# Performance work log

Measured on AMD Instinct MI355X. Metric: run time of the kernel, lower is better.

The kernel has to match this reference:

```python
import jax, jax.numpy as jnp
import numpy as np

NB_CLASSES = 10
EPS = 1e-8  # torch cosine_similarity eps


def gcn_conv(x, W, b, src, dst, n):
    h = x @ W
    deg = jax.ops.segment_sum(jnp.ones_like(src, dtype=h.dtype), dst, num_segments=n) + 1.0
    dinv = deg ** -0.5
    coef = (dinv[src] * dinv[dst])[:, None]
    agg = jax.ops.segment_sum(h[src] * coef, dst, num_segments=n)
    return agg + h * (1.0 / deg)[:, None] + b


def condition_net(e, w_in, b_in, w_hid, b_hid, w_out, b_out):
    # ConditionNet with num_layers=2: input_fc -> elu -> hidden_fc[0] -> elu -> output_fc
    h = jax.nn.elu(e @ w_in + b_in)
    h = jax.nn.elu(h @ w_hid + b_hid)
    return h @ w_out + b_out


def setup_inputs() -> dict:
    key = jax.random.key(0)
    N, E, D, H, T, M = 20000, 320000, 256, 256, 3, 2048
    ks = jax.random.split(key, 24)
    s = 1.0 / np.sqrt(D)
    inp = {
        "x": jax.random.normal(ks[0], (N, D), dtype=jnp.float32),
        "src": jax.random.randint(ks[1], (E,), 0, N, dtype=jnp.int32),
        "dst": jax.random.randint(ks[2], (E,), 0, N, dtype=jnp.int32),
        "idx": jax.random.randint(ks[3], (M,), 0, N, dtype=jnp.int32),
        "labels": jax.random.randint(ks[4], (M,), 0, NB_CLASSES, dtype=jnp.int32),
        "train": 1,
        # 3 GCNConv layers (all D->D, residual structure forces equal widths)
        "gcn_W1": jax.random.normal(ks[5], (D, D), dtype=jnp.float32) * s,
        "gcn_b1": jnp.zeros((D,), dtype=jnp.float32),
        "gcn_W2": jax.random.normal(ks[6], (D, D), dtype=jnp.float32) * s,
        "gcn_b2": jnp.zeros((D,), dtype=jnp.float32),
        "gcn_W3": jax.random.normal(ks[7], (D, D), dtype=jnp.float32) * s,
        "gcn_b3": jnp.zeros((D,), dtype=jnp.float32),
        # T=3 ConditionNets, params stacked on leading axis
        "cn_w_in": jax.random.normal(ks[8], (T, D, H), dtype=jnp.float32) * s,
        "cn_b_in": jnp.zeros((T, H), dtype=jnp.float32),
        "cn_w_hid": jax.random.normal(ks[9], (T, H, H), dtype=jnp.float32) * s,
        "cn_b_hid": jnp.zeros((T, H), dtype=jnp.float32),
        "cn_w_out": jax.random.normal(ks[10], (T, H, D), dtype=jnp.float32) * s,
        "cn_b_out": jnp.zeros((T, D), dtype=jnp.float32),
        # Embed_prompt
        "p_list": jax.random.normal(ks[11], (5, D), dtype=jnp.float32) * s,
        "a_W": jax.random.normal(ks[12], (D, 5), dtype=jnp.float32) * s,
        "a_b": jnp.zeros((5,), dtype=jnp.float32),
        # gcn_weight2 (trainable); weight1 and weight3 are frozen zeros, closed over
        "gcn_weight2": jnp.float32(1.0),
    }
    return inp


def reference(x, src, dst, idx, labels, train,
              gcn_W1, gcn_b1, gcn_W2, gcn_b2, gcn_W3, gcn_b3,
              cn_w_in, cn_b_in, cn_w_hid, cn_b_hid, cn_w_out, cn_b_out,
              p_list, a_W, a_b, gcn_weight2):
    n = x.shape[0]
    origin_x = x
    w1 = jnp.float32(0.0)  # gcn_weight1 (frozen)
    w3 = jnp.float32(0.0)  # gcn_weight3 (frozen)
    T = cn_w_in.shape[0]
    for t in range(T):  # think layers (small static count)
        e1 = gcn_conv(x, gcn_W1, gcn_b1, src, dst, n)
        e2 = gcn_conv(e1, gcn_W2, gcn_b2, src, dst, n) + e1
        e3 = gcn_conv(e2, gcn_W3, gcn_b3, src, dst, n) + e2
        embed = w1 * e1 + gcn_weight2 * e2 + w3 * e3
        prompt = condition_net(embed, cn_w_in[t], cn_b_in[t], cn_w_hid[t], cn_b_hid[t],
                               cn_w_out[t], cn_b_out[t])
        x = prompt * origin_x
    # full gcn(x, edge_index): 3 convs with ELU activation (standard GCN forward)
    h = jax.nn.elu(gcn_conv(x, gcn_W1, gcn_b1, src, dst, n))
    h = jax.nn.elu(gcn_conv(h, gcn_W2, gcn_b2, src, dst, n))
    h = jax.nn.elu(gcn_conv(h, gcn_W3, gcn_b3, src, dst, n))
    # Embed_prompt: attention over 5 learned prompt vectors
    weight = jax.nn.softmax(h @ a_W + a_b, axis=1)  # [N, 5]
    embed = h + weight @ p_list
    rawret = embed[idx]  # [M, D]
    # train==1: class prototypes via scatter-mean over labels
    sums = jax.ops.segment_sum(rawret, labels, num_segments=NB_CLASSES)
    counts = jax.ops.segment_sum(jnp.ones_like(labels, dtype=rawret.dtype), labels,
                                 num_segments=NB_CLASSES)
    ave = sums / jnp.maximum(counts, 1.0)[:, None]  # [C, D]
    # fused cosine similarity: normalize both, one matmul (replaces M*C scalar loop)
    rn = rawret / jnp.maximum(jnp.linalg.norm(rawret, axis=1, keepdims=True), EPS)
    an = ave / jnp.maximum(jnp.linalg.norm(ave, axis=1, keepdims=True), EPS)
    ret = jax.nn.softmax(rn @ an.T, axis=1)  # [M, C]
    return ret
```

## Files before the change

### kernel.cpp

```cpp
#include <hip/hip_runtime.h>
#include <hip/hip_bf16.h>
#include <math.h>

#define NN 20000
#define DD 256
#define EE 320000
#define MM 2048
#define CC 10
#define TT 3

typedef __attribute__((ext_vector_type(8))) short s8v;
typedef __attribute__((ext_vector_type(4))) float f4v;

__device__ unsigned short g_xb[NN * DD];
__device__ unsigned short g_xo[NN * DD];
__device__ unsigned short g_hb[NN * DD];
__device__ unsigned short g_e1b[NN * DD];
__device__ unsigned short g_e2b[NN * DD];
__device__ int   g_cnt[NN];
__device__ int   g_cursor[NN];
__device__ int   g_rowstart[NN + 1];
__device__ float g_dinv[NN];
__device__ float g_invdeg[NN];
__device__ int   g_part[128];
__device__ int2  g_edge[EE];
__device__ float g_sums[CC * DD];
__device__ float g_cntf[CC];
__device__ float g_an[CC * DD];
__device__ unsigned short g_wT1[12 * DD * DD];
__device__ unsigned short g_wT2[12 * DD * DD];

__device__ __forceinline__ float wave_sum(float v) {
#pragma unroll
  for (int off = 32; off > 0; off >>= 1) v += __shfl_xor(v, off);
  return v;
}

__device__ __forceinline__ float eluf(float x) {
  return x > 0.f ? x : expm1f(x);
}

__device__ __forceinline__ float bf2f(unsigned short u) {
  union { unsigned int i; float f; } c;
  c.i = (unsigned int)u << 16;
  return c.f;
}

__device__ __forceinline__ float2 bfpair(unsigned int d) {
  union { unsigned int i; float f; } a, b;
  a.i = d << 16;
  b.i = d & 0xffff0000u;
  return make_float2(a.f, b.f);
}

__device__ __forceinline__ unsigned int packbf(float x, float y) {
  union { __hip_bfloat162 v; unsigned int u; } c;
  c.v = __float22bfloat162_rn(make_float2(x, y));
  return c.u;
}

__device__ __forceinline__ void gl_lds16(const unsigned short* g, unsigned short* l) {
  __builtin_amdgcn_global_load_lds(
      (const __attribute__((address_space(1))) unsigned int*)g,
      (__attribute__((address_space(3))) unsigned int*)l, 16, 0, 0);
}

__global__ void zero_pre() {
  int i = blockIdx.x * blockDim.x + threadIdx.x;
  if (i < NN) { g_cnt[i] = 0; g_cursor[i] = 0; }
  if (i < CC * DD) g_sums[i] = 0.f;
  if (i < CC) g_cntf[i] = 0.f;
}

__global__ void hist_k(const int* __restrict__ dst) {
  int e = blockIdx.x * blockDim.x + threadIdx.x;
  if (e < EE) atomicAdd(&g_cnt[dst[e]], 1);
}

__global__ __launch_bounds__(256) void scanA_k() {
  __shared__ int s[256];
  int t = threadIdx.x;
  int i = blockIdx.x * 256 + t;
  int v = (i < NN) ? g_cnt[i] : 0;
  s[t] = v;
  __syncthreads();
#pragma unroll
  for (int off = 128; off > 0; off >>= 1) {
    if (t < off) s[t] += s[t + off];
    __syncthreads();
  }
  if (t == 0) g_part[blockIdx.x] = s[0];
}

__global__ __launch_bounds__(128) void scanB_k() {
  __shared__ int s[128];
  int t = threadIdx.x;
  int p = (t < 79) ? g_part[t] : 0;
  s[t] = p;
  __syncthreads();
#pragma unroll
  for (int off = 1; off < 128; off <<= 1) {
    int v = (t >= off) ? s[t - off] : 0;
    __syncthreads();
    s[t] += v;
    __syncthreads();
  }
  g_part[t] = s[t] - p;
  if (t == 0) g_rowstart[NN] = EE;
}

__global__ __launch_bounds__(256) void scanC_k() {
  __shared__ int s[256];
  int t = threadIdx.x;
  int i = blockIdx.x * 256 + t;
  int v = (i < NN) ? g_cnt[i] : 0;
  s[t] = v;
  __syncthreads();
#pragma unroll
  for (int off = 1; off < 256; off <<= 1) {
    int x = (t >= off) ? s[t - off] : 0;
    __syncthreads();
    s[t] += x;
    __syncthreads();
  }
  if (i < NN) {
    g_rowstart[i] = g_part[blockIdx.x] + s[t] - v;
    float dg = (float)(v + 1);
    g_invdeg[i] = 1.0f / dg;
    g_dinv[i] = 1.0f / sqrtf(dg);
  }
}

__global__ void fill_k(const int* __restrict__ src, const int* __restrict__ dst) {
  int e = blockIdx.x * blockDim.x + threadIdx.x;
  if (e < EE) {
    int d = dst[e];
    int p = atomicAdd(&g_cursor[d], 1);
    int j = g_rowstart[d] + p;
    int si = src[e];
    float coef = g_dinv[si] * g_dinv[d];
    g_edge[j] = make_int2(si * 512, __float_as_int(coef));
  }
}

__global__ __launch_bounds__(256) void cvt_k(const float* __restrict__ x,
                                             unsigned short* __restrict__ xb) {
  int i = blockIdx.x * blockDim.x + threadIdx.x;
  const float4* x4 = (const float4*)x;
  float4 a = x4[i * 2], b = x4[i * 2 + 1];
  uint4 o;
  o.x = packbf(a.x, a.y);
  o.y = packbf(a.z, a.w);
  o.z = packbf(b.x, b.y);
  o.w = packbf(b.z, b.w);
  ((uint4*)xb)[i] = o;
}

struct WPtrs { const float* p[12]; };

__global__ __launch_bounds__(256) void wprep_k(WPtrs wp) {
  __shared__ float t[64][65];
  int widx = blockIdx.z;
  int kt0 = blockIdx.x * 64, nt0 = blockIdx.y * 64;
  const float* W = wp.p[widx];
  int tid = threadIdx.x;
  int ln = tid & 63, lk = tid >> 6;
  for (int kk = lk; kk < 64; kk += 4)
    t[kk][ln] = W[(size_t)(kt0 + kk) * DD + nt0 + ln];
  __syncthreads();
  for (int nn = lk; nn < 64; nn += 4) {
    float v = t[ln][nn];
    __hip_bfloat16 hb = __float2bfloat16(v);
    float hf = __bfloat162float(hb);
    __hip_bfloat16 lb = __float2bfloat16(v - hf);
    union { __hip_bfloat16 b; unsigned short s; } ch, cl;
    ch.b = hb; cl.b = lb;
    size_t o = (size_t)widx * DD * DD + (size_t)(nt0 + nn) * DD + kt0 + ln;
    g_wT1[o] = ch.s;
    g_wT2[o] = cl.s;
  }
}

template <int SPLIT>
union GemmSM {
  unsigned short st[2][(1024 + 512 * SPLIT) * 8];
  float ct[64][68];
};

template <int EPI, int SPLIT>
__global__ __launch_bounds__(256) void gemm_k(const unsigned short* __restrict__ A,
                                              const unsigned short* __restrict__ B1,
                                              const unsigned short* __restrict__ B2,
                                              unsigned short* __restrict__ C,
                                              const float* __restrict__ bias,
                                              const float* __restrict__ alphap,
                                              const unsigned short* __restrict__ mul) {
  __shared__ GemmSM<SPLIT> sm;
  constexpr int CB = 1024 + 512 * SPLIT;
  int b = blockIdx.x;
  int xcd = b & 7, off = b >> 3;
  int logical = (xcd < 4) ? xcd * 157 + off : 628 + (xcd - 4) * 156 + off;
  int mblk = logical >> 2, nblk = logical & 3;
  int row0 = mblk * 64, col0 = nblk * 64;

  int tid = threadIdx.x;
  int wv = tid >> 6, lane = tid & 63;
  int wm = wv >> 1, wn = wv & 1;
  int lr = lane & 15, lk = lane >> 4;

  f4v acc[2][2];
#pragma unroll
  for (int i = 0; i < 2; ++i)
#pragma unroll
    for (int j = 0; j < 2; ++j) acc[i][j] = (f4v){0.f, 0.f, 0.f, 0.f};

  auto stage = [&](int buf, int kt) {
    unsigned short* base = sm.st[buf];
#pragma unroll
    for (int i = 0; i < CB / 256; ++i) {
      int cb = (wv * (CB / 256) + i) * 64;
      int c = cb + lane;
      unsigned short* ldst = base + (size_t)cb * 8;
      if (c < 512) {
        int row = c >> 3, pos = c & 7;
        int kc = pos ^ (row & 7);
        int gr = row0 + row;
        gr = gr < NN ? gr : NN - 1;
        gl_lds16(A + (size_t)gr * DD + kt + kc * 8, ldst);
      } else if (c < 1024) {
        int c2 = c - 512;
        int col = c2 >> 3, pos = c2 & 7;
        int kc = pos ^ (col & 7);
        gl_lds16(B1 + (size_t)(col0 + col) * DD + kt + kc * 8, ldst);
      } else {
        int c2 = c - 1024;
        int col = c2 >> 3, pos = c2 & 7;
        int kc = pos ^ (col & 7);
        gl_lds16(B2 + (size_t)(col0 + col) * DD + kt + kc * 8, ldst);
      }
    }
  };

  stage(0, 0);
  __syncthreads();

  int buf = 0;
#pragma unroll
  for (int t = 0; t < 4; ++t) {
    if (t < 3) stage(buf ^ 1, (t + 1) * 64);
    const unsigned short* base = sm.st[buf];
#pragma unroll
    for (int ksub = 0; ksub < 2; ++ksub) {
      int kc = ksub * 4 + lk;
      s8v a[2], b1v[2], b2v[2];
#pragma unroll
      for (int mi = 0; mi < 2; ++mi) {
        int row = wm * 32 + mi * 16 + lr;
        a[mi] = *(const s8v*)(base + (row * 8 + (kc ^ (row & 7))) * 8);
      }
#pragma unroll
      for (int nj = 0; nj < 2; ++nj) {
        int col = wn * 32 + nj * 16 + lr;
        int ch = col * 8 + (kc ^ (col & 7));
        b1v[nj] = *(const s8v*)(base + (512 + ch) * 8);
        if (SPLIT) b2v[nj] = *(const s8v*)(base + (1024 + ch) * 8);
      }
#pragma unroll
      for (int mi = 0; mi < 2; ++mi)
#pragma unroll
        for (int nj = 0; nj < 2; ++nj) {
          acc[mi][nj] = __builtin_amdgcn_mfma_f32_16x16x32_bf16(a[mi], b1v[nj], acc[mi][nj], 0, 0, 0);
          if (SPLIT)
            acc[mi][nj] = __builtin_amdgcn_mfma_f32_16x16x32_bf16(a[mi], b2v[nj], acc[mi][nj], 0, 0, 0);
        }
    }
    __syncthreads();
    buf ^= 1;
  }

#pragma unroll
  for (int mi = 0; mi < 2; ++mi)
#pragma unroll
    for (int nj = 0; nj < 2; ++nj)
#pragma unroll
      for (int r = 0; r < 4; ++r)
        sm.ct[wm * 32 + mi * 16 + lk * 4 + r][wn * 32 + nj * 16 + lr] = acc[mi][nj][r];
  __syncthreads();

  float alpha = 1.f;
  if (EPI == 1) alpha = alphap ? *alphap : 1.f;
#pragma unroll
  for (int p = 0; p < 2; ++p) {
    int row = p * 32 + (tid >> 3);
    int c0 = (tid & 7) * 8;
    int gr = row0 + row;
    int gc = col0 + c0;
    if (gr < NN) {
      float v[8];
      float4 va = *(float4*)&sm.ct[row][c0];
      float4 vb = *(float4*)&sm.ct[row][c0 + 4];
      v[0] = va.x; v[1] = va.y; v[2] = va.z; v[3] = va.w;
      v[4] = vb.x; v[5] = vb.y; v[6] = vb.z; v[7] = vb.w;
      if (EPI == 1) {
        float4 bv0 = *(const float4*)(bias + gc);
        float4 bv1 = *(const float4*)(bias + gc + 4);
        float bb[8] = {bv0.x, bv0.y, bv0.z, bv0.w, bv1.x, bv1.y, bv1.z, bv1.w};
#pragma unroll
        for (int i = 0; i < 8; ++i) v[i] = eluf(fmaf(alpha, v[i], bb[i]));
      } else if (EPI == 2) {
        float4 bv0 = *(const float4*)(bias + gc);
        float4 bv1 = *(const float4*)(bias + gc + 4);
        float bb[8] = {bv0.x, bv0.y, bv0.z, bv0.w, bv1.x, bv1.y, bv1.z, bv1.w};
        uint4 mu = *(const uint4*)(mul + (size_t)gr * DD + gc);
        float2 m0 = bfpair(mu.x), m1 = bfpair(mu.y), m2 = bfpair(mu.z), m3 = bfpair(mu.w);
        float mm[8] = {m0.x, m0.y, m1.x, m1.y, m2.x, m2.y, m3.x, m3.y};
#pragma unroll
        for (int i = 0; i < 8; ++i) v[i] = (v[i] + bb[i]) * mm[i];
      }
      uint4 o;
      o.x = packbf(v[0], v[1]);
      o.y = packbf(v[2], v[3]);
      o.z = packbf(v[4], v[5]);
      o.w = packbf(v[6], v[7]);
      *(uint4*)(C + (size_t)gr * DD + gc) = o;
    }
  }
}

template <int RES>
__device__ __forceinline__ float4 agg_row_b(int row, int lane,
                                            const unsigned short* __restrict__ h,
                                            const float* __restrict__ bias,
                                            const unsigned short* __restrict__ res) {
  const char* hb = (const char*)h;
  int lo = lane * 8;
  float4 a = make_float4(0.f, 0.f, 0.f, 0.f);
  int s = g_rowstart[row], e = g_rowstart[row + 1];
  int j = s;
  for (; j + 16 <= e; j += 16) {
    int2 E[16];
    uint2 v[16];
#pragma unroll
    for (int u = 0; u < 16; ++u) E[u] = g_edge[j + u];
#pragma unroll
    for (int u = 0; u < 16; ++u) v[u] = *(const uint2*)(hb + E[u].x + lo);
#pragma unroll
    for (int u = 0; u < 16; ++u) {
      float c = __int_as_float(E[u].y);
      float2 p0 = bfpair(v[u].x), p1 = bfpair(v[u].y);
      a.x = fmaf(c, p0.x, a.x); a.y = fmaf(c, p0.y, a.y);
      a.z = fmaf(c, p1.x, a.z); a.w = fmaf(c, p1.y, a.w);
    }
  }
  for (; j + 4 <= e; j += 4) {
    int2 E[4];
    uint2 v[4];
#pragma unroll
    for (int u = 0; u < 4; ++u) E[u] = g_edge[j + u];
#pragma unroll
    for (int u = 0; u < 4; ++u) v[u] = *(const uint2*)(hb + E[u].x + lo);
#pragma unroll
    for (int u = 0; u < 4; ++u) {
      float c = __int_as_float(E[u].y);
      float2 p0 = bfpair(v[u].x), p1 = bfpair(v[u].y);
      a.x = fmaf(c, p0.x, a.x); a.y = fmaf(c, p0.y, a.y);
      a.z = fmaf(c, p1.x, a.z); a.w = fmaf(c, p1.y, a.w);
    }
  }
  for (; j < e; ++j) {
    int2 E0 = g_edge[j];
    uint2 v0 = *(const uint2*)(hb + E0.x + lo);
    float c = __int_as_float(E0.y);
    float2 p0 = bfpair(v0.x), p1 = bfpair(v0.y);
    a.x = fmaf(c, p0.x, a.x); a.y = fmaf(c, p0.y, a.y);
    a.z = fmaf(c, p1.x, a.z); a.w = fmaf(c, p1.y, a.w);
  }
  float idg = g_invdeg[row];
  uint2 hv = *(const uint2*)(hb + row * 512 + lo);
  float2 h0 = bfpair(hv.x), h1 = bfpair(hv.y);
  float4 bv = ((const float4*)bias)[lane];
  float4 o;
  o.x = a.x + h0.x * idg + bv.x;
  o.y = a.y + h0.y * idg + bv.y;
  o.z = a.z + h1.x * idg + bv.z;
  o.w = a.w + h1.y * idg + bv.w;
  if (RES) {
    uint2 rv = *(const uint2*)((const char*)res + row * 512 + lo);
    float2 r0 = bfpair(rv.x), r1 = bfpair(rv.y);
    o.x += r0.x; o.y += r0.y; o.z += r1.x; o.w += r1.y;
  }
  return o;
}

template <int ELU, int RES>
__global__ __launch_bounds__(256) void agg_k(const unsigned short* __restrict__ h,
                                             const float* __restrict__ bias,
                                             const unsigned short* __restrict__ res,
                                             unsigned short* __restrict__ out) {
  int row = (blockIdx.x * 256 + threadIdx.x) >> 6;
  int lane = threadIdx.x & 63;
  float4 o = agg_row_b<RES>(row, lane, h, bias, res);
  if (ELU) {
    o.x = eluf(o.x); o.y = eluf(o.y); o.z = eluf(o.z); o.w = eluf(o.w);
  }
  ((uint2*)out)[(size_t)row * 64 + lane] = make_uint2(packbf(o.x, o.y), packbf(o.z, o.w));
}

__global__ __launch_bounds__(256) void aggattn_k(const unsigned short* __restrict__ h,
                                                 const float* __restrict__ bias,
                                                 const float* __restrict__ aW,
                                                 const float* __restrict__ ab,
                                                 const float* __restrict__ plist,
                                                 unsigned short* __restrict__ out) {
  int row = (blockIdx.x * 256 + threadIdx.x) >> 6;
  int lane = threadIdx.x & 63;
  float4 o = agg_row_b<0>(row, lane, h, bias, nullptr);
  o.x = eluf(o.x); o.y = eluf(o.y); o.z = eluf(o.z); o.w = eluf(o.w);
  int d = lane * 4;
  float lg[5];
#pragma unroll
  for (int k = 0; k < 5; ++k) {
    float p = o.x * aW[(d + 0) * 5 + k] + o.y * aW[(d + 1) * 5 + k] +
              o.z * aW[(d + 2) * 5 + k] + o.w * aW[(d + 3) * 5 + k];
    lg[k] = wave_sum(p) + ab[k];
  }
  float mx = lg[0];
#pragma unroll
  for (int k = 1; k < 5; ++k) mx = fmaxf(mx, lg[k]);
  float w[5], sum = 0.f;
#pragma unroll
  for (int k = 0; k < 5; ++k) { w[k] = expf(lg[k] - mx); sum += w[k]; }
  float inv = 1.f / sum;
#pragma unroll
  for (int k = 0; k < 5; ++k) {
    float wk = w[k] * inv;
    float4 pv = ((const float4*)plist)[k * 64 + lane];
    o.x = fmaf(wk, pv.x, o.x);
    o.y = fmaf(wk, pv.y, o.y);
    o.z = fmaf(wk, pv.z, o.z);
    o.w = fmaf(wk, pv.w, o.w);
  }
  ((uint2*)out)[(size_t)row * 64 + lane] = make_uint2(packbf(o.x, o.y), packbf(o.z, o.w));
}

__global__ __launch_bounds__(256) void proto_k(const unsigned short* __restrict__ embed,
                                               const int* __restrict__ idxp,
                                               const int* __restrict__ labels) {
  __shared__ float sums[CC][DD];
  __shared__ float cnts[CC];
  int t = threadIdx.x;
#pragma unroll
  for (int c = 0; c < CC; ++c) sums[c][t] = 0.f;
  if (t < CC) cnts[t] = 0.f;
  __syncthreads();
  int m0 = blockIdx.x * 32;
  for (int r0 = 0; r0 < 32; r0 += 4) {
    int i4[4], l4[4];
    float v[4];
#pragma unroll
    for (int u = 0; u < 4; ++u) {
      int m = m0 + r0 + u;
      i4[u] = idxp[m];
      l4[u] = labels[m];
    }
#pragma unroll
    for (int u = 0; u < 4; ++u) v[u] = bf2f(embed[(size_t)i4[u] * DD + t]);
#pragma unroll
    for (int u = 0; u < 4; ++u) sums[l4[u]][t] += v[u];
    if (t == 0) {
#pragma unroll
      for (int u = 0; u < 4; ++u) cnts[l4[u]] += 1.f;
    }
  }
  __syncthreads();
#pragma unroll
  for (int c = 0; c < CC; ++c) atomicAdd(&g_sums[c * DD + t], sums[c][t]);
  if (t < CC) atomicAdd(&g_cntf[t], cnts[t]);
}

__global__ void protonorm_k() {
  __shared__ float red[4];
  int t = threadIdx.x;
  int lane = t & 63, w = t >> 6;
  for (int c = 0; c < CC; ++c) {
    float v = g_sums[c * DD + t] / fmaxf(g_cntf[c], 1.0f);
    float sq = wave_sum(v * v);
    if (lane == 0) red[w] = sq;
    __syncthreads();
    float tot = red[0] + red[1] + red[2] + red[3];
    float nrm = fmaxf(sqrtf(tot), 1e-8f);
    g_an[c * DD + t] = v / nrm;
    __syncthreads();
  }
}

__global__ __launch_bounds__(256) void cos_k(const unsigned short* __restrict__ embed,
                                             const int* __restrict__ idxp,
                                             float* __restrict__ out) {
  int wid = (blockIdx.x * 256 + threadIdx.x) >> 6;
  int lane = threadIdx.x & 63;
  if (wid >= MM) return;
  int row = idxp[wid];
  uint2 rv = ((const uint2*)embed)[(size_t)row * 64 + lane];
  float2 r0 = bfpair(rv.x), r1 = bfpair(rv.y);
  float4 r = make_float4(r0.x, r0.y, r1.x, r1.y);
  float n = wave_sum(r.x * r.x + r.y * r.y + r.z * r.z + r.w * r.w);
  float rnf = 1.0f / fmaxf(sqrtf(n), 1e-8f);
  float lg[CC];
#pragma unroll
  for (int c = 0; c < CC; ++c) {
    float4 a = ((const float4*)g_an)[c * 64 + lane];
    float p = r.x * a.x + r.y * a.y + r.z * a.z + r.w * a.w;
    lg[c] = wave_sum(p) * rnf;
  }
  float mx = lg[0];
#pragma unroll
  for (int c = 1; c < CC; ++c) mx = fmaxf(mx, lg[c]);
  float s = 0.f, w[CC];
#pragma unroll
  for (int c = 0; c < CC; ++c) { w[c] = expf(lg[c] - mx); s += w[c]; }
  float inv = 1.f / s;
#pragma unroll
  for (int c = 0; c < CC; ++c)
    if (lane == c) out[(size_t)wid * CC + c] = w[c] * inv;
}

extern "C" void kernel_launch(void* const* d_in, const int* in_sizes, int n_in,
                              void* d_out, int out_size, void* d_ws, size_t ws_size,
                              hipStream_t stream) {
  (void)in_sizes; (void)n_in; (void)d_ws; (void)ws_size; (void)out_size;
  const float* x      = (const float*)d_in[0];
  const int*   src    = (const int*)d_in[1];
  const int*   dst    = (const int*)d_in[2];
  const int*   idx    = (const int*)d_in[3];
  const int*   labels = (const int*)d_in[4];
  const float* W1 = (const float*)d_in[6];
  const float* b1 = (const float*)d_in[7];
  const float* W2 = (const float*)d_in[8];
  const float* b2 = (const float*)d_in[9];
  const float* W3 = (const float*)d_in[10];
  const float* b3 = (const float*)d_in[11];
  const float* cw_in  = (const float*)d_in[12];
  const float* cb_in  = (const float*)d_in[13];
  const float* cw_hid = (const float*)d_in[14];
  const float* cb_hid = (const float*)d_in[15];
  const float* cw_out = (const float*)d_in[16];
  const float* cb_out = (const float*)d_in[17];
  const float* plist  = (const float*)d_in[18];
  const float* aW     = (const float*)d_in[19];
  const float* ab     = (const float*)d_in[20];
  const float* w2s    = (const float*)d_in[21];
  float* out = (float*)d_out;

  unsigned short *xb, *xo, *hb, *e1b, *e2b, *wt1, *wt2;
  hipGetSymbolAddress((void**)&xb,  HIP_SYMBOL(g_xb));
  hipGetSymbolAddress((void**)&xo,  HIP_SYMBOL(g_xo));
  hipGetSymbolAddress((void**)&hb,  HIP_SYMBOL(g_hb));
  hipGetSymbolAddress((void**)&e1b, HIP_SYMBOL(g_e1b));
  hipGetSymbolAddress((void**)&e2b, HIP_SYMBOL(g_e2b));
  hipGetSymbolAddress((void**)&wt1, HIP_SYMBOL(g_wT1));
  hipGetSymbolAddress((void**)&wt2, HIP_SYMBOL(g_wT2));

  auto WT1 = [&](int w) { return (const unsigned short*)(wt1 + (size_t)w * DD * DD); };
  auto WT2 = [&](int w) { return (const unsigned short*)(wt2 + (size_t)w * DD * DD); };

  zero_pre<<<79, 256, 0, stream>>>();
  hist_k<<<1250, 256, 0, stream>>>(dst);
  scanA_k<<<79, 256, 0, stream>>>();
  scanB_k<<<1, 128, 0, stream>>>();
  scanC_k<<<79, 256, 0, stream>>>();
  fill_k<<<1250, 256, 0, stream>>>(src, dst);
  cvt_k<<<2500, 256, 0, stream>>>(x, xb);

  WPtrs wp;
  wp.p[0] = W1; wp.p[1] = W2; wp.p[2] = W3;
  for (int t = 0; t < 3; ++t) {
    wp.p[3 + t] = cw_in  + (size_t)t * DD * DD;
    wp.p[6 + t] = cw_hid + (size_t)t * DD * DD;
    wp.p[9 + t] = cw_out + (size_t)t * DD * DD;
  }
  wprep_k<<<dim3(4, 4, 12), 256, 0, stream>>>(wp);

  const int GG = 1252;
  const unsigned short* xin = xb;
  for (int t = 0; t < TT; ++t) {
    gemm_k<0, 1><<<GG, 256, 0, stream>>>(xin, WT1(0), WT2(0), hb, nullptr, nullptr, nullptr);
    agg_k<0, 0><<<5000, 256, 0, stream>>>(hb, b1, nullptr, e1b);
    gemm_k<0, 1><<<GG, 256, 0, stream>>>(e1b, WT1(1), WT2(1), hb, nullptr, nullptr, nullptr);
    agg_k<0, 1><<<5000, 256, 0, stream>>>(hb, b2, e1b, e2b);
    gemm_k<1, 0><<<GG, 256, 0, stream>>>(e2b, WT1(3 + t), WT1(3 + t), e1b,
                                         cb_in + (size_t)t * DD, w2s, nullptr);
    gemm_k<1, 0><<<GG, 256, 0, stream>>>(e1b, WT1(6 + t), WT1(6 + t), hb,
                                         cb_hid + (size_t)t * DD, nullptr, nullptr);
    gemm_k<2, 0><<<GG, 256, 0, stream>>>(hb, WT1(9 + t), WT1(9 + t), xo,
                                         cb_out + (size_t)t * DD, nullptr, xb);
    xin = xo;
  }

  gemm_k<0, 1><<<GG, 256, 0, stream>>>(xin, WT1(0), WT2(0), hb, nullptr, nullptr, nullptr);
  agg_k<1, 0><<<5000, 256, 0, stream>>>(hb, b1, nullptr, e1b);
  gemm_k<0, 1><<<GG, 256, 0, stream>>>(e1b, WT1(1), WT2(1), hb, nullptr, nullptr, nullptr);
  agg_k<1, 0><<<5000, 256, 0, stream>>>(hb, b2, nullptr, e2b);
  gemm_k<0, 1><<<GG, 256, 0, stream>>>(e2b, WT1(2), WT2(2), hb, nullptr, nullptr, nullptr);
  aggattn_k<<<5000, 256, 0, stream>>>(hb, b3, aW, ab, plist, e2b);

  proto_k<<<64, 256, 0, stream>>>(e2b, idx, labels);
  protonorm_k<<<1, 256, 0, stream>>>();
  cos_k<<<512, 256, 0, stream>>>(e2b, idx, out);
}
```

Before: 579.8 us.

## Fuse setup kernels, fold scan and protonorm, widen aggregation gathers to 16 bytes

Merges the zero, bf16 conversion and weight-prep kernels into one init kernel. It folds the single-block partial-sum scan into scanC and the prototype normalization into cos_k, which cuts several launches. The SpMM aggregation now splits each wave into two half-waves that each gather 16-byte row slices for alternating edges and combine them with a shuffle, so each load is wider and half as many row segments are fetched per lane. Each cos block recomputes the prototype norms redundantly, and the odd-edge tail uses a clamped index with a zero coefficient.

```diff
diff --git a/kernel.cpp b/kernel.cpp
--- a/kernel.cpp
+++ b/kernel.cpp
@@ -26,7 +26,6 @@
 __device__ int2  g_edge[EE];
 __device__ float g_sums[CC * DD];
 __device__ float g_cntf[CC];
-__device__ float g_an[CC * DD];
 __device__ unsigned short g_wT1[12 * DD * DD];
 __device__ unsigned short g_wT2[12 * DD * DD];
 
@@ -65,11 +64,51 @@
       (__attribute__((address_space(3))) unsigned int*)l, 16, 0, 0);
 }
 
-__global__ void zero_pre() {
-  int i = blockIdx.x * blockDim.x + threadIdx.x;
-  if (i < NN) { g_cnt[i] = 0; g_cursor[i] = 0; }
-  if (i < CC * DD) g_sums[i] = 0.f;
-  if (i < CC) g_cntf[i] = 0.f;
+struct WPtrs { const float* p[12]; };
+
+__global__ __launch_bounds__(256) void init_k(const float* __restrict__ x,
+                                              unsigned short* __restrict__ xb,
+                                              WPtrs wp) {
+  __shared__ float t[64][65];
+  int b = blockIdx.x;
+  int tid = threadIdx.x;
+  if (b < 2500) {
+    int i = b * 256 + tid;
+    const float4* x4 = (const float4*)x;
+    float4 a = x4[i * 2], bb = x4[i * 2 + 1];
+    uint4 o;
+    o.x = packbf(a.x, a.y);
+    o.y = packbf(a.z, a.w);
+    o.z = packbf(bb.x, bb.y);
+    o.w = packbf(bb.z, bb.w);
+    ((uint4*)xb)[i] = o;
+  } else if (b < 2692) {
+    int bb = b - 2500;
+    int widx = bb >> 4;
+    int rem = bb & 15;
+    int kt0 = (rem >> 2) * 64, nt0 = (rem & 3) * 64;
+    const float* W = wp.p[widx];
+    int ln = tid & 63, lk = tid >> 6;
+    for (int kk = lk; kk < 64; kk += 4)
+      t[kk][ln] = W[(size_t)(kt0 + kk) * DD + nt0 + ln];
+    __syncthreads();
+    for (int nn = lk; nn < 64; nn += 4) {
+      float v = t[ln][nn];
+      __hip_bfloat16 hb = __float2bfloat16(v);
+      float hf = __bfloat162float(hb);
+      __hip_bfloat16 lb = __float2bfloat16(v - hf);
+      union { __hip_bfloat16 b; unsigned short s; } ch, cl;
+      ch.b = hb; cl.b = lb;
+      size_t o = (size_t)widx * DD * DD + (size_t)(nt0 + nn) * DD + kt0 + ln;
+      g_wT1[o] = ch.s;
+      g_wT2[o] = cl.s;
+    }
+  } else {
+    int i = (b - 2692) * 256 + tid;
+    if (i < NN) { g_cnt[i] = 0; g_cursor[i] = 0; }
+    if (i < CC * DD) g_sums[i] = 0.f;
+    if (i < CC) g_cntf[i] = 0.f;
+  }
 }
 
 __global__ void hist_k(const int* __restrict__ dst) {
@@ -92,43 +131,38 @@
   if (t == 0) g_part[blockIdx.x] = s[0];
 }
 
-__global__ __launch_bounds__(128) void scanB_k() {
-  __shared__ int s[128];
-  int t = threadIdx.x;
-  int p = (t < 79) ? g_part[t] : 0;
-  s[t] = p;
-  __syncthreads();
-#pragma unroll
-  for (int off = 1; off < 128; off <<= 1) {
-    int v = (t >= off) ? s[t - off] : 0;
-    __syncthreads();
-    s[t] += v;
-    __syncthreads();
-  }
-  g_part[t] = s[t] - p;
-  if (t == 0) g_rowstart[NN] = EE;
-}
-
 __global__ __launch_bounds__(256) void scanC_k() {
+  __shared__ int ps[128];
   __shared__ int s[256];
   int t = threadIdx.x;
+  if (t < 128) ps[t] = (t < 79) ? g_part[t] : 0;
+  __syncthreads();
+#pragma unroll
+  for (int off = 1; off < 128; off <<= 1) {
+    int v = (t >= off && t < 128) ? ps[t - off] : 0;
+    __syncthreads();
+    if (t < 128) ps[t] += v;
+    __syncthreads();
+  }
+  int base = (blockIdx.x == 0) ? 0 : ps[blockIdx.x - 1];
   int i = blockIdx.x * 256 + t;
   int v = (i < NN) ? g_cnt[i] : 0;
   s[t] = v;
   __syncthreads();
 #pragma unroll
   for (int off = 1; off < 256; off <<= 1) {
-    int x = (t >= off) ? s[t - off] : 0;
-    __syncthreads();
-    s[t] += x;
+    int x2 = (t >= off) ? s[t - off] : 0;
+    __syncthreads();
+    s[t] += x2;
     __syncthreads();
   }
   if (i < NN) {
-    g_rowstart[i] = g_part[blockIdx.x] + s[t] - v;
+    g_rowstart[i] = base + s[t] - v;
     float dg = (float)(v + 1);
     g_invdeg[i] = 1.0f / dg;
     g_dinv[i] = 1.0f / sqrtf(dg);
   }
+  if (blockIdx.x == 78 && t == 0) g_rowstart[NN] = EE;
 }
 
 __global__ void fill_k(const int* __restrict__ src, const int* __restrict__ dst) {
@@ -140,44 +174,6 @@
     int si = src[e];
     float coef = g_dinv[si] * g_dinv[d];
     g_edge[j] = make_int2(si * 512, __float_as_int(coef));
-  }
-}
-
-__global__ __launch_bounds__(256) void cvt_k(const float* __restrict__ x,
-                                             unsigned short* __restrict__ xb) {
-  int i = blockIdx.x * blockDim.x + threadIdx.x;
-  const float4* x4 = (const float4*)x;
-  float4 a = x4[i * 2], b = x4[i * 2 + 1];
-  uint4 o;
-  o.x = packbf(a.x, a.y);
-  o.y = packbf(a.z, a.w);
-  o.z = packbf(b.x, b.y);
-  o.w = packbf(b.z, b.w);
-  ((uint4*)xb)[i] = o;
-}
-
-struct WPtrs { const float* p[12]; };
-
-__global__ __launch_bounds__(256) void wprep_k(WPtrs wp) {
-  __shared__ float t[64][65];
-  int widx = blockIdx.z;
-  int kt0 = blockIdx.x * 64, nt0 = blockIdx.y * 64;
-  const float* W = wp.p[widx];
-  int tid = threadIdx.x;
-  int ln = tid & 63, lk = tid >> 6;
-  for (int kk = lk; kk < 64; kk += 4)
-    t[kk][ln] = W[(size_t)(kt0 + kk) * DD + nt0 + ln];
-  __syncthreads();
-  for (int nn = lk; nn < 64; nn += 4) {
-    float v = t[ln][nn];
-    __hip_bfloat16 hb = __float2bfloat16(v);
-    float hf = __bfloat162float(hb);
-    __hip_bfloat16 lb = __float2bfloat16(v - hf);
-    union { __hip_bfloat16 b; unsigned short s; } ch, cl;
-    ch.b = hb; cl.b = lb;
-    size_t o = (size_t)widx * DD * DD + (size_t)(nt0 + nn) * DD + kt0 + ln;
-    g_wT1[o] = ch.s;
-    g_wT2[o] = cl.s;
   }
 }
 
@@ -328,68 +324,67 @@
 }
 
 template <int RES>
-__device__ __forceinline__ float4 agg_row_b(int row, int lane,
-                                            const unsigned short* __restrict__ h,
-                                            const float* __restrict__ bias,
-                                            const unsigned short* __restrict__ res) {
+__device__ __forceinline__ void agg_row8(int row, int sl, int hf,
+                                         const unsigned short* __restrict__ h,
+                                         const float* __restrict__ bias,
+                                         const unsigned short* __restrict__ res,
+                                         float* o) {
   const char* hb = (const char*)h;
-  int lo = lane * 8;
-  float4 a = make_float4(0.f, 0.f, 0.f, 0.f);
+  int lo = sl * 16;
+  float acc[8];
+#pragma unroll
+  for (int k = 0; k < 8; ++k) acc[k] = 0.f;
   int s = g_rowstart[row], e = g_rowstart[row + 1];
   int j = s;
-  for (; j + 16 <= e; j += 16) {
-    int2 E[16];
-    uint2 v[16];
-#pragma unroll
-    for (int u = 0; u < 16; ++u) E[u] = g_edge[j + u];
-#pragma unroll
-    for (int u = 0; u < 16; ++u) v[u] = *(const uint2*)(hb + E[u].x + lo);
-#pragma unroll
-    for (int u = 0; u < 16; ++u) {
+  for (; j + 12 <= e; j += 12) {
+    int2 E[6];
+    uint4 V[6];
+#pragma unroll
+    for (int u = 0; u < 6; ++u) E[u] = g_edge[j + 2 * u + hf];
+#pragma unroll
+    for (int u = 0; u < 6; ++u) V[u] = *(const uint4*)(hb + (size_t)E[u].x + lo);
+#pragma unroll
+    for (int u = 0; u < 6; ++u) {
       float c = __int_as_float(E[u].y);
-      float2 p0 = bfpair(v[u].x), p1 = bfpair(v[u].y);
-      a.x = fmaf(c, p0.x, a.x); a.y = fmaf(c, p0.y, a.y);
-      a.z = fmaf(c, p1.x, a.z); a.w = fmaf(c, p1.y, a.w);
+      float2 p0 = bfpair(V[u].x), p1 = bfpair(V[u].y);
+      float2 p2 = bfpair(V[u].z), p3 = bfpair(V[u].w);
+      acc[0] = fmaf(c, p0.x, acc[0]); acc[1] = fmaf(c, p0.y, acc[1]);
+      acc[2] = fmaf(c, p1.x, acc[2]); acc[3] = fmaf(c, p1.y, acc[3]);
+      acc[4] = fmaf(c, p2.x, acc[4]); acc[5] = fmaf(c, p2.y, acc[5]);
+      acc[6] = fmaf(c, p3.x, acc[6]); acc[7] = fmaf(c, p3.y, acc[7]);
     }
   }
-  for (; j + 4 <= e; j += 4) {
-    int2 E[4];
-    uint2 v[4];
-#pragma unroll
-    for (int u = 0; u < 4; ++u) E[u] = g_edge[j + u];
-#pragma unroll
-    for (int u = 0; u < 4; ++u) v[u] = *(const uint2*)(hb + E[u].x + lo);
-#pragma unroll
-    for (int u = 0; u < 4; ++u) {
-      float c = __int_as_float(E[u].y);
-      float2 p0 = bfpair(v[u].x), p1 = bfpair(v[u].y);
-      a.x = fmaf(c, p0.x, a.x); a.y = fmaf(c, p0.y, a.y);
-      a.z = fmaf(c, p1.x, a.z); a.w = fmaf(c, p1.y, a.w);
-    }
-  }
-  for (; j < e; ++j) {
-    int2 E0 = g_edge[j];
-    uint2 v0 = *(const uint2*)(hb + E0.x + lo);
-    float c = __int_as_float(E0.y);
-    float2 p0 = bfpair(v0.x), p1 = bfpair(v0.y);
-    a.x = fmaf(c, p0.x, a.x); a.y = fmaf(c, p0.y, a.y);
-    a.z = fmaf(c, p1.x, a.z); a.w = fmaf(c, p1.y, a.w);
-  }
+  for (; j < e; j += 2) {
+    int jj = j + hf;
+    int jc = jj < e ? jj : e - 1;
+    int2 E0 = g_edge[jc];
+    uint4 V0 = *(const uint4*)(hb + (size_t)E0.x + lo);
+    float c = (jj < e) ? __int_as_float(E0.y) : 0.f;
+    float2 p0 = bfpair(V0.x), p1 = bfpair(V0.y);
+    float2 p2 = bfpair(V0.z), p3 = bfpair(V0.w);
+    acc[0] = fmaf(c, p0.x, acc[0]); acc[1] = fmaf(c, p0.y, acc[1]);
+    acc[2] = fmaf(c, p1.x, acc[2]); acc[3] = fmaf(c, p1.y, acc[3]);
+    acc[4] = fmaf(c, p2.x, acc[4]); acc[5] = fmaf(c, p2.y, acc[5]);
+    acc[6] = fmaf(c, p3.x, acc[6]); acc[7] = fmaf(c, p3.y, acc[7]);
+  }
+#pragma unroll
+  for (int k = 0; k < 8; ++k) acc[k] += __shfl_xor(acc[k], 32);
   float idg = g_invdeg[row];
-  uint2 hv = *(const uint2*)(hb + row * 512 + lo);
-  float2 h0 = bfpair(hv.x), h1 = bfpair(hv.y);
-  float4 bv = ((const float4*)bias)[lane];
-  float4 o;
-  o.x = a.x + h0.x * idg + bv.x;
-  o.y = a.y + h0.y * idg + bv.y;
-  o.z = a.z + h1.x * idg + bv.z;
-  o.w = a.w + h1.y * idg + bv.w;
+  uint4 hv = *(const uint4*)(hb + (size_t)row * 512 + lo);
+  float2 h0 = bfpair(hv.x), h1 = bfpair(hv.y), h2 = bfpair(hv.z), h3 = bfpair(hv.w);
+  float hw[8] = {h0.x, h0.y, h1.x, h1.y, h2.x, h2.y, h3.x, h3.y};
+  float4 b0 = *(const float4*)(bias + sl * 8);
+  float4 b1 = *(const float4*)(bias + sl * 8 + 4);
+  float bb[8] = {b0.x, b0.y, b0.z, b0.w, b1.x, b1.y, b1.z, b1.w};
+#pragma unroll
+  for (int k = 0; k < 8; ++k) o[k] = acc[k] + hw[k] * idg + bb[k];
   if (RES) {
-    uint2 rv = *(const uint2*)((const char*)res + row * 512 + lo);
-    float2 r0 = bfpair(rv.x), r1 = bfpair(rv.y);
-    o.x += r0.x; o.y += r0.y; o.z += r1.x; o.w += r1.y;
-  }
-  return o;
+    uint4 rv = *(const uint4*)((const char*)res + (size_t)row * 512 + lo);
+    float2 r0 = bfpair(rv.x), r1 = bfpair(rv.y), r2 = bfpair(rv.z), r3 = bfpair(rv.w);
+    float rw[8] = {r0.x, r0.y, r1.x, r1.y, r2.x, r2.y, r3.x, r3.y};
+#pragma unroll
+    for (int k = 0; k < 8; ++k) o[k] += rw[k];
+  }
 }
 
 template <int ELU, int RES>
@@ -399,11 +394,21 @@
                                              unsigned short* __restrict__ out) {
   int row = (blockIdx.x * 256 + threadIdx.x) >> 6;
   int lane = threadIdx.x & 63;
-  float4 o = agg_row_b<RES>(row, lane, h, bias, res);
+  int sl = lane & 31, hf = lane >> 5;
+  float o[8];
+  agg_row8<RES>(row, sl, hf, h, bias, res, o);
   if (ELU) {
-    o.x = eluf(o.x); o.y = eluf(o.y); o.z = eluf(o.z); o.w = eluf(o.w);
-  }
-  ((uint2*)out)[(size_t)row * 64 + lane] = make_uint2(packbf(o.x, o.y), packbf(o.z, o.w));
+#pragma unroll
+    for (int k = 0; k < 8; ++k) o[k] = eluf(o[k]);
+  }
+  if (hf == 0) {
+    uint4 pk;
+    pk.x = packbf(o[0], o[1]);
+    pk.y = packbf(o[2], o[3]);
+    pk.z = packbf(o[4], o[5]);
+    pk.w = packbf(o[6], o[7]);
+    *(uint4*)((char*)out + (size_t)row * 512 + sl * 16) = pk;
+  }
 }
 
 __global__ __launch_bounds__(256) void aggattn_k(const unsigned short* __restrict__ h,
@@ -414,15 +419,19 @@
                                                  unsigned short* __restrict__ out) {
   int row = (blockIdx.x * 256 + threadIdx.x) >> 6;
   int lane = threadIdx.x & 63;
-  float4 o = agg_row_b<0>(row, lane, h, bias, nullptr);
-  o.x = eluf(o.x); o.y = eluf(o.y); o.z = eluf(o.z); o.w = eluf(o.w);
-  int d = lane * 4;
+  int sl = lane & 31, hf = lane >> 5;
+  float o[8];
+  agg_row8<0>(row, sl, hf, h, bias, nullptr, o);
+#pragma unroll
+  for (int k = 0; k < 8; ++k) o[k] = eluf(o[k]);
+  int c0 = sl * 8;
   float lg[5];
 #pragma unroll
   for (int k = 0; k < 5; ++k) {
-    float p = o.x * aW[(d + 0) * 5 + k] + o.y * aW[(d + 1) * 5 + k] +
-              o.z * aW[(d + 2) * 5 + k] + o.w * aW[(d + 3) * 5 + k];
-    lg[k] = wave_sum(p) + ab[k];
+    float p = 0.f;
+#pragma unroll
+    for (int i = 0; i < 8; ++i) p = fmaf(o[i], aW[(c0 + i) * 5 + k], p);
+    lg[k] = wave_sum(p) * 0.5f + ab[k];
   }
   float mx = lg[0];
 #pragma unroll
@@ -434,13 +443,21 @@
 #pragma unroll
   for (int k = 0; k < 5; ++k) {
     float wk = w[k] * inv;
-    float4 pv = ((const float4*)plist)[k * 64 + lane];
-    o.x = fmaf(wk, pv.x, o.x);
-    o.y = fmaf(wk, pv.y, o.y);
-    o.z = fmaf(wk, pv.z, o.z);
-    o.w = fmaf(wk, pv.w, o.w);
-  }
-  ((uint2*)out)[(size_t)row * 64 + lane] = make_uint2(packbf(o.x, o.y), packbf(o.z, o.w));
+    float4 p0 = *(const float4*)(plist + k * DD + c0);
+    float4 p1 = *(const float4*)(plist + k * DD + c0 + 4);
+    o[0] = fmaf(wk, p0.x, o[0]); o[1] = fmaf(wk, p0.y, o[1]);
+    o[2] = fmaf(wk, p0.z, o[2]); o[3] = fmaf(wk, p0.w, o[3]);
+    o[4] = fmaf(wk, p1.x, o[4]); o[5] = fmaf(wk, p1.y, o[5]);
+    o[6] = fmaf(wk, p1.z, o[6]); o[7] = fmaf(wk, p1.w, o[7]);
+  }
+  if (hf == 0) {
+    uint4 pk;
+    pk.x = packbf(o[0], o[1]);
+    pk.y = packbf(o[2], o[3]);
+    pk.z = packbf(o[4], o[5]);
+    pk.w = packbf(o[6], o[7]);
+    *(uint4*)((char*)out + (size_t)row * 512 + sl * 16) = pk;
+  }
 }
 
 __global__ __launch_bounds__(256) void proto_k(const unsigned short* __restrict__ embed,
@@ -478,27 +495,24 @@
   if (t < CC) atomicAdd(&g_cntf[t], cnts[t]);
 }
 
-__global__ void protonorm_k() {
+__global__ __launch_bounds__(256) void cos_k(const unsigned short* __restrict__ embed,
+                                             const int* __restrict__ idxp,
+                                             float* __restrict__ out) {
+  __shared__ float an[CC][DD];
   __shared__ float red[4];
   int t = threadIdx.x;
-  int lane = t & 63, w = t >> 6;
+  int lane = t & 63, wv = t >> 6;
   for (int c = 0; c < CC; ++c) {
     float v = g_sums[c * DD + t] / fmaxf(g_cntf[c], 1.0f);
     float sq = wave_sum(v * v);
-    if (lane == 0) red[w] = sq;
+    if (lane == 0) red[wv] = sq;
     __syncthreads();
     float tot = red[0] + red[1] + red[2] + red[3];
     float nrm = fmaxf(sqrtf(tot), 1e-8f);
-    g_an[c * DD + t] = v / nrm;
-    __syncthreads();
-  }
-}
-
-__global__ __launch_bounds__(256) void cos_k(const unsigned short* __restrict__ embed,
-                                             const int* __restrict__ idxp,
-                                             float* __restrict__ out) {
-  int wid = (blockIdx.x * 256 + threadIdx.x) >> 6;
-  int lane = threadIdx.x & 63;
+    an[c][t] = v / nrm;
+    __syncthreads();
+  }
+  int wid = (blockIdx.x * 256 + t) >> 6;
   if (wid >= MM) return;
   int row = idxp[wid];
   uint2 rv = ((const uint2*)embed)[(size_t)row * 64 + lane];
@@ -509,7 +523,7 @@
   float lg[CC];
 #pragma unroll
   for (int c = 0; c < CC; ++c) {
-    float4 a = ((const float4*)g_an)[c * 64 + lane];
+    float4 a = ((const float4*)&an[c][0])[lane];
     float p = r.x * a.x + r.y * a.y + r.z * a.z + r.w * a.w;
     lg[c] = wave_sum(p) * rnf;
   }
@@ -564,14 +578,6 @@
   auto WT1 = [&](int w) { return (const unsigned short*)(wt1 + (size_t)w * DD * DD); };
   auto WT2 = [&](int w) { return (const unsigned short*)(wt2 + (size_t)w * DD * DD); };
 
-  zero_pre<<<79, 256, 0, stream>>>();
-  hist_k<<<1250, 256, 0, stream>>>(dst);
-  scanA_k<<<79, 256, 0, stream>>>();
-  scanB_k<<<1, 128, 0, stream>>>();
-  scanC_k<<<79, 256, 0, stream>>>();
-  fill_k<<<1250, 256, 0, stream>>>(src, dst);
-  cvt_k<<<2500, 256, 0, stream>>>(x, xb);
-
   WPtrs wp;
   wp.p[0] = W1; wp.p[1] = W2; wp.p[2] = W3;
   for (int t = 0; t < 3; ++t) {
@@ -579,7 +585,11 @@
     wp.p[6 + t] = cw_hid + (size_t)t * DD * DD;
     wp.p[9 + t] = cw_out + (size_t)t * DD * DD;
   }
-  wprep_k<<<dim3(4, 4, 12), 256, 0, stream>>>(wp);
+  init_k<<<2771, 256, 0, stream>>>(x, xb, wp);
+  hist_k<<<1250, 256, 0, stream>>>(dst);
+  scanA_k<<<79, 256, 0, stream>>>();
+  scanC_k<<<79, 256, 0, stream>>>();
+  fill_k<<<1250, 256, 0, stream>>>(src, dst);
 
   const int GG = 1252;
   const unsigned short* xin = xb;
@@ -605,6 +615,5 @@
   aggattn_k<<<5000, 256, 0, stream>>>(hb, b3, aW, ab, plist, e2b);
 
   proto_k<<<64, 256, 0, stream>>>(e2b, idx, labels);
-  protonorm_k<<<1, 256, 0, stream>>>();
   cos_k<<<512, 256, 0, stream>>>(e2b, idx, out);
 }
```

Measured after the change: 539.3 us. 7.0% less time.
